# Optimization experiments

Hardware: AMD Instinct MI355X
Metric: run time of the kernel (lower is better)

## Reference

```python
import jax, jax.numpy as jnp
import numpy as np

H = 4        # nhead
TEMP = 0.1   # temperature
TOP_K = 5
SHAPE_EPS = 1e-5


def _ln(x, g, b):
    m = x.mean(-1, keepdims=True)
    v = ((x - m) ** 2).mean(-1, keepdims=True)
    return (x - m) / jnp.sqrt(v + SHAPE_EPS) * g + b


def _mha(x, Wqkv, bqkv, Wo, bo):
    B, L, D = x.shape
    Dh = D // H
    qkv = x @ Wqkv.T + bqkv                     # [B,L,3D]
    q, k, v = jnp.split(qkv, 3, axis=-1)
    q = q.reshape(B, L, H, Dh)
    k = k.reshape(B, L, H, Dh)
    v = v.reshape(B, L, H, Dh)
    att = jnp.einsum('bqhd,bkhd->bhqk', q, k) * (1.0 / np.sqrt(Dh))
    att = jax.nn.softmax(att, axis=-1)
    o = jnp.einsum('bhqk,bkhd->bqhd', att, v).reshape(B, L, D)
    return o @ Wo.T + bo


def _pattern_encoder(x, cls_token, Wqkv, bqkv, Wo, bo, ln1_g, ln1_b,
                     W1, b1, W2, b2, ln2_g, ln2_b, proj_W, proj_b, proj_g, proj_bb):
    B, L, D = x.shape
    h = jnp.concatenate([jnp.broadcast_to(cls_token, (B, 1, D)), x], axis=1)  # [B,L+1,D]
    for i in range(Wqkv.shape[0]):  # num_layers=2, post-norm (PyTorch default)
        a = _mha(h, Wqkv[i], bqkv[i], Wo[i], bo[i])
        h = _ln(h + a, ln1_g[i], ln1_b[i])
        f = jax.nn.gelu(h @ W1[i].T + b1[i], approximate=False) @ W2[i].T + b2[i]
        h = _ln(h + f, ln2_g[i], ln2_b[i])
    cls_out = h[:, 0, :]
    return _ln(cls_out @ proj_W.T + proj_b, proj_g, proj_bb)  # [B,d_repr]


def _value_encoder(xm, vW1, vb1, v_g, v_b, vW2, vb2):
    hh = _ln(xm @ vW1.T + vb1, v_g, v_b)
    return jax.nn.gelu(hh, approximate=False) @ vW2.T + vb2


def setup_inputs() -> dict:
    B, L, D, DR, N, P, NL = 64, 512, 512, 128, 10000, 96, 2
    key = jax.random.key(0)
    ks = jax.random.split(key, 16)
    sc = 0.02
    inp = {
        'query': jax.random.normal(ks[0], (B, L, D), jnp.float32),
        'memory_keys': jax.random.normal(ks[1], (N, DR), jnp.float32),
        'memory_values': jax.random.normal(ks[2], (N, P, D), jnp.float32),
        'cls_token': jax.random.normal(ks[3], (1, 1, D), jnp.float32) * sc,
        'Wqkv': jax.random.normal(ks[4], (NL, 3 * D, D), jnp.float32) * sc,
        'bqkv': jnp.zeros((NL, 3 * D), jnp.float32),
        'Wo': jax.random.normal(ks[5], (NL, D, D), jnp.float32) * sc,
        'bo': jnp.zeros((NL, D), jnp.float32),
        'ln1_g': jnp.ones((NL, D), jnp.float32),
        'ln1_b': jnp.zeros((NL, D), jnp.float32),
        'W1': jax.random.normal(ks[6], (NL, 2 * D, D), jnp.float32) * sc,
        'b1': jnp.zeros((NL, 2 * D), jnp.float32),
        'W2': jax.random.normal(ks[7], (NL, D, 2 * D), jnp.float32) * sc,
        'b2': jnp.zeros((NL, D), jnp.float32),
        'ln2_g': jnp.ones((NL, D), jnp.float32),
        'ln2_b': jnp.zeros((NL, D), jnp.float32),
        'proj_W': jax.random.normal(ks[8], (DR, D), jnp.float32) * sc,
        'proj_b': jnp.zeros((DR,), jnp.float32),
        'proj_g': jnp.ones((DR,), jnp.float32),
        'proj_bb': jnp.zeros((DR,), jnp.float32),
        'vW1': jax.random.normal(ks[9], (DR, D), jnp.float32) * sc,
        'vb1': jnp.zeros((DR,), jnp.float32),
        'v_g': jnp.ones((DR,), jnp.float32),
        'v_b': jnp.zeros((DR,), jnp.float32),
        'vW2': jax.random.normal(ks[10], (DR, DR), jnp.float32) * sc,
        'vb2': jnp.zeros((DR,), jnp.float32),
        'shape_w': jnp.float32(0.5),
    }
    return inp


def reference(query, memory_keys, memory_values, cls_token, Wqkv, bqkv, Wo, bo,
              ln1_g, ln1_b, W1, b1, W2, b2, ln2_g, ln2_b,
              proj_W, proj_b, proj_g, proj_bb, vW1, vb1, v_g, v_b, vW2, vb2, shape_w):
    q_repr = _pattern_encoder(query, cls_token, Wqkv, bqkv, Wo, bo, ln1_g, ln1_b,
                              W1, b1, W2, b2, ln2_g, ln2_b, proj_W, proj_b, proj_g, proj_bb)
    q_val = _value_encoder(query.mean(axis=1), vW1, vb1, v_g, v_b, vW2, vb2)
    qk = shape_w * q_repr + (1.0 - shape_w) * q_val              # [B,DR]
    # squared euclidean distance, expanded form (same math as sum((a-b)^2))
    d = ((qk ** 2).sum(-1)[:, None]
         - 2.0 * qk @ memory_keys.T
         + (memory_keys ** 2).sum(-1)[None, :])                  # [B,N]
    sim = -d / TEMP
    top_scores, top_idx = jax.lax.top_k(sim, TOP_K)              # [B,K]
    weights = jax.nn.softmax(top_scores, axis=-1)
    retrieved = memory_values[top_idx]                           # [B,K,P,D]
    return retrieved, weights
```

## Files before the change

kernel.cpp:

```cpp
#include <hip/hip_runtime.h>
#include <math.h>

#define B_    64
#define LQ    512
#define LC    513
#define DD    512
#define HH    4
#define DH    128
#define DRr   128
#define NKEYS 10000
#define PP    96
#define TOPK  5
#define MROWS (B_*LC)
#define VTSTRIDE 544

typedef __attribute__((ext_vector_type(8))) short short8v;
typedef __attribute__((ext_vector_type(4))) float f32x4;

static __device__ __forceinline__ float gelu_exact(float x) {
    return 0.5f * x * (1.0f + erff(x * 0.70710678118654752440f));
}

static __device__ __forceinline__ unsigned short f2bf(float x) {
    union { float f; unsigned u; } v; v.f = x;
    unsigned r = v.u + 0x7fff + ((v.u >> 16) & 1);
    return (unsigned short)(r >> 16);
}
static __device__ __forceinline__ float bf2f(unsigned short h) {
    union { float f; unsigned u; } v; v.u = ((unsigned)h) << 16;
    return v.f;
}
static __device__ __forceinline__ void split_bf(float x, unsigned short& hi, unsigned short& lo) {
    hi = f2bf(x);
    lo = f2bf(x - bf2f(hi));
}

static __device__ __forceinline__ void gload16(const unsigned short* g, unsigned short* l) {
    __builtin_amdgcn_global_load_lds(
        (const __attribute__((address_space(1))) unsigned*)g,
        (__attribute__((address_space(3))) unsigned*)l, 16, 0, 0);
}

__global__ __launch_bounds__(256)
void split_kernel(const float* __restrict__ x, unsigned short* __restrict__ hi,
                  unsigned short* __restrict__ lo, int n4)
{
    int i = blockIdx.x * blockDim.x + threadIdx.x;
    if (i >= n4) return;
    float4 v = ((const float4*)x)[i];
    unsigned short h0,h1,h2,h3,l0,l1,l2,l3;
    split_bf(v.x,h0,l0); split_bf(v.y,h1,l1); split_bf(v.z,h2,l2); split_bf(v.w,h3,l3);
    ((uint2*)hi)[i] = make_uint2((unsigned)h0 | ((unsigned)h1 << 16), (unsigned)h2 | ((unsigned)h3 << 16));
    ((uint2*)lo)[i] = make_uint2((unsigned)l0 | ((unsigned)l1 << 16), (unsigned)l2 | ((unsigned)l3 << 16));
}

__global__ __launch_bounds__(128)
void concat_cls(const float* __restrict__ query, const float* __restrict__ cls,
                float* __restrict__ h, unsigned short* __restrict__ h_hi,
                unsigned short* __restrict__ h_lo)
{
    int row = blockIdx.x;
    int t = threadIdx.x;
    int b = row / LC, r = row - b * LC;
    const float* src = (r == 0) ? cls : (query + ((size_t)b * LQ + (r - 1)) * DD);
    float4 v = *(const float4*)(src + t * 4);
    *(float4*)(h + (size_t)row * DD + t * 4) = v;
    unsigned short hs[4], ls[4];
    split_bf(v.x, hs[0], ls[0]); split_bf(v.y, hs[1], ls[1]);
    split_bf(v.z, hs[2], ls[2]); split_bf(v.w, hs[3], ls[3]);
    size_t o = (size_t)row * DD + t * 4;
    ((uint2*)(h_hi))[o >> 2] = make_uint2((unsigned)hs[0] | ((unsigned)hs[1]<<16),
                                          (unsigned)hs[2] | ((unsigned)hs[3]<<16));
    ((uint2*)(h_lo))[o >> 2] = make_uint2((unsigned)ls[0] | ((unsigned)ls[1]<<16),
                                          (unsigned)ls[2] | ((unsigned)ls[3]<<16));
}

#define BM 128
#define BN 128
#define BK 32

#define MFMA16(a, b, c) __builtin_amdgcn_mfma_f32_16x16x32_bf16(a, b, c, 0, 0, 0)

template<int MODE>
__global__ __launch_bounds__(256)
void gemm3(const unsigned short* __restrict__ Ahi, const unsigned short* __restrict__ Alo,
           const unsigned short* __restrict__ Whi, const unsigned short* __restrict__ Wlo,
           const float* __restrict__ bias, const float* __restrict__ res,
           float* __restrict__ Cf, unsigned short* __restrict__ Chi,
           unsigned short* __restrict__ Clo, unsigned short* __restrict__ Vhi,
           unsigned short* __restrict__ Vlo, int M, int N, int K)
{
    __shared__ __align__(16) unsigned short LAh[4096];
    __shared__ __align__(16) unsigned short LAl[4096];
    __shared__ __align__(16) unsigned short LBh[4096];
    __shared__ __align__(16) unsigned short LBl[4096];

    const int t = threadIdx.x;
    const int lane = t & 63, w = t >> 6;
    const int wr = w >> 1, wc = w & 1;
    const int row0 = blockIdx.x * BM, col0 = blockIdx.y * BN;

    const int srow = t >> 2;
    const int sg   = t & 3;
    const int glog = sg ^ ((srow >> 1) & 3);
    int ar0 = row0 + srow;      if (ar0 >= M) ar0 = M - 1;
    int ar1 = row0 + srow + 64; if (ar1 >= M) ar1 = M - 1;
    const size_t aoff0 = (size_t)ar0 * K + glog * 8;
    const size_t aoff1 = (size_t)ar1 * K + glog * 8;
    const size_t boff0 = (size_t)(col0 + srow) * K + glog * 8;
    const size_t boff1 = (size_t)(col0 + srow + 64) * K + glog * 8;
    const int ldso0 = t * 8;
    const int ldso1 = t * 8 + 2048;

    f32x4 acc[4][4];
    #pragma unroll
    for (int m = 0; m < 4; m++)
        #pragma unroll
        for (int n = 0; n < 4; n++) { acc[m][n][0]=0.f; acc[m][n][1]=0.f; acc[m][n][2]=0.f; acc[m][n][3]=0.f; }

    const int c = lane & 15;
    const int g = lane >> 4;
    const int gs = (g ^ ((c >> 1) & 3)) * 8;

    const int KT = K / BK;
    for (int kt = 0; kt < KT; kt++) {
        const int k0 = kt * BK;
        __syncthreads();
        gload16(Ahi + aoff0 + k0, &LAh[ldso0]);
        gload16(Ahi + aoff1 + k0, &LAh[ldso1]);
        gload16(Alo + aoff0 + k0, &LAl[ldso0]);
        gload16(Alo + aoff1 + k0, &LAl[ldso1]);
        gload16(Whi + boff0 + k0, &LBh[ldso0]);
        gload16(Whi + boff1 + k0, &LBh[ldso1]);
        gload16(Wlo + boff0 + k0, &LBl[ldso0]);
        gload16(Wlo + boff1 + k0, &LBl[ldso1]);
        __syncthreads();

        short8v ah[4], al[4], bh[4], bl[4];
        #pragma unroll
        for (int m = 0; m < 4; m++) {
            int off = (wr * 64 + m * 16 + c) * 32 + gs;
            ah[m] = *(const short8v*)&LAh[off];
            al[m] = *(const short8v*)&LAl[off];
        }
        #pragma unroll
        for (int n = 0; n < 4; n++) {
            int off = (wc * 64 + n * 16 + c) * 32 + gs;
            bh[n] = *(const short8v*)&LBh[off];
            bl[n] = *(const short8v*)&LBl[off];
        }

        #pragma unroll
        for (int m = 0; m < 4; m++)
            #pragma unroll
            for (int n = 0; n < 4; n++) {
                acc[m][n] = MFMA16(ah[m], bh[n], acc[m][n]);
                acc[m][n] = MFMA16(al[m], bh[n], acc[m][n]);
                acc[m][n] = MFMA16(ah[m], bl[n], acc[m][n]);
            }
    }

    #pragma unroll
    for (int m = 0; m < 4; m++) {
        int rb = row0 + wr * 64 + m * 16 + (lane >> 4) * 4;
        #pragma unroll
        for (int n = 0; n < 4; n++) {
            int cc = col0 + wc * 64 + n * 16 + c;
            float bcol = bias[cc];
            #pragma unroll
            for (int r = 0; r < 4; r++) {
                int row = rb + r;
                if (row < M) {
                    float v = acc[m][n][r] + bcol;
                    if (MODE == 1) v += res[(size_t)row * N + cc];
                    if (MODE == 2) {
                        v = gelu_exact(v);
                        unsigned short hv, lv;
                        split_bf(v, hv, lv);
                        Chi[(size_t)row * N + cc] = hv;
                        Clo[(size_t)row * N + cc] = lv;
                    } else if (MODE == 3) {
                        unsigned short hv, lv;
                        split_bf(v, hv, lv);
                        if (cc < 1024) {
                            Chi[(size_t)row * 1024 + cc] = hv;
                            Clo[(size_t)row * 1024 + cc] = lv;
                        } else {
                            int da = cc - 1024, hh = da >> 7, dd = da & 127;
                            int bb = row / LC, ll = row - bb * LC;
                            size_t vi = ((size_t)((bb * HH + hh) * DH + dd)) * VTSTRIDE + ll;
                            Vhi[vi] = hv; Vlo[vi] = lv;
                        }
                    } else {
                        Cf[(size_t)row * N + cc] = v;
                    }
                }
            }
        }
    }
}

#define AQT 64
#define AKT 32
#define NKT2 17
__global__ __launch_bounds__(256)
void attn_mfma(const unsigned short* __restrict__ qkhi, const unsigned short* __restrict__ qklo,
               const unsigned short* __restrict__ vthi, const unsigned short* __restrict__ vtlo,
               unsigned short* __restrict__ ohi, unsigned short* __restrict__ olo)
{
    __shared__ __align__(16) unsigned short SM[24064];
    #define KH(r,d) SM[(r)*136 + (d)]
    #define KL(r,d) SM[4352 + (r)*136 + (d)]
    #define VH(d,k) SM[8704 + (d)*40 + (k)]
    #define VL(d,k) SM[13824 + (d)*40 + (k)]
    #define PH(r,k) SM[18944 + (r)*40 + (k)]
    #define PL(r,k) SM[21504 + (r)*40 + (k)]
    #define OS(r,d) SM[(r)*136 + (d)]

    const int t = threadIdx.x;
    const int lane = t & 63, w = t >> 6;
    const int qt = blockIdx.x, h = blockIdx.y, b = blockIdx.z;
    const int q0 = qt * AQT;
    const int c = lane & 15, g = lane >> 4;
    const float SCALE = 0.08838834764831845f;

    short8v qh[4], ql[4];
    {
        int qrow = b * LC + q0 + w * 16 + c;
        if (qrow > MROWS - 1) qrow = MROWS - 1;
        const unsigned short* bh_ = qkhi + (size_t)qrow * 1024 + h * DH;
        const unsigned short* bl_ = qklo + (size_t)qrow * 1024 + h * DH;
        #pragma unroll
        for (int ks = 0; ks < 4; ks++) {
            qh[ks] = *(const short8v*)(bh_ + ks * 32 + g * 8);
            ql[ks] = *(const short8v*)(bl_ + ks * 32 + g * 8);
        }
    }

    float m_r[4], l_r[4];
    #pragma unroll
    for (int r = 0; r < 4; r++) { m_r[r] = -INFINITY; l_r[r] = 0.f; }
    f32x4 acc_o[8];
    #pragma unroll
    for (int n = 0; n < 8; n++) { acc_o[n][0]=0.f; acc_o[n][1]=0.f; acc_o[n][2]=0.f; acc_o[n][3]=0.f; }

    const int skr = t >> 3, skd = (t & 7) * 16;
    const int svd = t >> 1, svk = (t & 1) * 16;

    for (int kt = 0; kt < NKT2; kt++) {
        __syncthreads();
        {
            int krow = b * LC + kt * AKT + skr;
            if (krow > MROWS - 1) krow = MROWS - 1;
            const unsigned short* kb  = qkhi + (size_t)krow * 1024 + 512 + h * DH + skd;
            const unsigned short* kbl = qklo + (size_t)krow * 1024 + 512 + h * DH + skd;
            *(short8v*)&KH(skr, skd)     = *(const short8v*)kb;
            *(short8v*)&KH(skr, skd + 8) = *(const short8v*)(kb + 8);
            *(short8v*)&KL(skr, skd)     = *(const short8v*)kbl;
            *(short8v*)&KL(skr, skd + 8) = *(const short8v*)(kbl + 8);
            const unsigned short* vb  = vthi + ((size_t)((b * HH + h) * DH + svd)) * VTSTRIDE + kt * AKT + svk;
            const unsigned short* vbl = vtlo + ((size_t)((b * HH + h) * DH + svd)) * VTSTRIDE + kt * AKT + svk;
            *(short8v*)&VH(svd, svk)     = *(const short8v*)vb;
            *(short8v*)&VH(svd, svk + 8) = *(const short8v*)(vb + 8);
            *(short8v*)&VL(svd, svk)     = *(const short8v*)vbl;
            *(short8v*)&VL(svd, svk + 8) = *(const short8v*)(vbl + 8);
        }
        __syncthreads();

        f32x4 s[2];
        s[0][0]=s[0][1]=s[0][2]=s[0][3]=0.f;
        s[1][0]=s[1][1]=s[1][2]=s[1][3]=0.f;
        #pragma unroll
        for (int n = 0; n < 2; n++) {
            #pragma unroll
            for (int ks = 0; ks < 4; ks++) {
                short8v kh = *(const short8v*)&KH(n * 16 + c, ks * 32 + g * 8);
                short8v kl = *(const short8v*)&KL(n * 16 + c, ks * 32 + g * 8);
                s[n] = MFMA16(qh[ks], kh, s[n]);
                s[n] = MFMA16(ql[ks], kh, s[n]);
                s[n] = MFMA16(qh[ks], kl, s[n]);
            }
        }

        #pragma unroll
        for (int n = 0; n < 2; n++) {
            bool oob = (kt * 32 + n * 16 + c) >= LC;
            #pragma unroll
            for (int r = 0; r < 4; r++) {
                float sv = s[n][r] * SCALE;
                s[n][r] = oob ? -INFINITY : sv;
            }
        }

        float alpha[4], p0v[4], p1v[4];
        #pragma unroll
        for (int r = 0; r < 4; r++) {
            float rm = fmaxf(s[0][r], s[1][r]);
            #pragma unroll
            for (int off = 1; off < 16; off <<= 1) rm = fmaxf(rm, __shfl_xor(rm, off));
            float mn = fmaxf(m_r[r], rm);
            float p0 = expf(s[0][r] - mn);
            float p1 = expf(s[1][r] - mn);
            float ts = p0 + p1;
            #pragma unroll
            for (int off = 1; off < 16; off <<= 1) ts += __shfl_xor(ts, off);
            float al = expf(m_r[r] - mn);
            m_r[r] = mn;
            l_r[r] = al * l_r[r] + ts;
            alpha[r] = al;
            p0v[r] = p0; p1v[r] = p1;
        }

        #pragma unroll
        for (int n = 0; n < 8; n++)
            #pragma unroll
            for (int r = 0; r < 4; r++) acc_o[n][r] *= alpha[r];

        #pragma unroll
        for (int r = 0; r < 4; r++) {
            unsigned short ph, pl;
            split_bf(p0v[r], ph, pl);
            PH(w * 16 + g * 4 + r, c) = ph;
            PL(w * 16 + g * 4 + r, c) = pl;
            split_bf(p1v[r], ph, pl);
            PH(w * 16 + g * 4 + r, 16 + c) = ph;
            PL(w * 16 + g * 4 + r, 16 + c) = pl;
        }
        __syncthreads();

        short8v pah = *(const short8v*)&PH(w * 16 + c, g * 8);
        short8v pal = *(const short8v*)&PL(w * 16 + c, g * 8);
        #pragma unroll
        for (int n = 0; n < 8; n++) {
            short8v vh = *(const short8v*)&VH(n * 16 + c, g * 8);
            short8v vl = *(const short8v*)&VL(n * 16 + c, g * 8);
            acc_o[n] = MFMA16(pah, vh, acc_o[n]);
            acc_o[n] = MFMA16(pal, vh, acc_o[n]);
            acc_o[n] = MFMA16(pah, vl, acc_o[n]);
        }
    }

    float inv[4];
    #pragma unroll
    for (int r = 0; r < 4; r++) inv[r] = 1.0f / l_r[r];

    const int orow = t >> 2, oc0 = (t & 3) * 32;
    #pragma unroll
    for (int pass = 0; pass < 2; pass++) {
        __syncthreads();
        #pragma unroll
        for (int n = 0; n < 8; n++)
            #pragma unroll
            for (int r = 0; r < 4; r++) {
                float v = acc_o[n][r] * inv[r];
                unsigned short hv, lv;
                split_bf(v, hv, lv);
                OS(w * 16 + g * 4 + r, n * 16 + c) = pass ? lv : hv;
            }
        __syncthreads();
        int grow = q0 + orow;
        if (grow < LC) {
            unsigned short* dst = (pass ? olo : ohi) + ((size_t)(b * LC + grow)) * DD + h * DH + oc0;
            #pragma unroll
            for (int u = 0; u < 4; u++)
                *(short8v*)(dst + u * 8) = *(const short8v*)&OS(orow, oc0 + u * 8);
        }
    }
    #undef KH
    #undef KL
    #undef VH
    #undef VL
    #undef PH
    #undef PL
    #undef OS
}

__global__ __launch_bounds__(128)
void ln512(const float* __restrict__ X, const float* __restrict__ g,
           const float* __restrict__ bb, float* __restrict__ Y,
           unsigned short* __restrict__ Yhi, unsigned short* __restrict__ Ylo)
{
    __shared__ float red[2];
    int row = blockIdx.x, t = threadIdx.x;
    const float* x = X + (size_t)row * DD;
    float4 v = *(const float4*)(x + t * 4);
    float s = v.x + v.y + v.z + v.w;
    #pragma unroll
    for (int off = 1; off < 64; off <<= 1) s += __shfl_xor(s, off);
    if ((t & 63) == 0) red[t >> 6] = s;
    __syncthreads();
    float mean = (red[0] + red[1]) * (1.0f / 512.0f);
    __syncthreads();
    float d0 = v.x - mean, d1 = v.y - mean, d2 = v.z - mean, d3 = v.w - mean;
    float s2 = d0 * d0 + d1 * d1 + d2 * d2 + d3 * d3;
    #pragma unroll
    for (int off = 1; off < 64; off <<= 1) s2 += __shfl_xor(s2, off);
    if ((t & 63) == 0) red[t >> 6] = s2;
    __syncthreads();
    float var = (red[0] + red[1]) * (1.0f / 512.0f);
    float rstd = 1.0f / sqrtf(var + 1e-5f);
    float4 gv = *(const float4*)(g + t * 4);
    float4 bv = *(const float4*)(bb + t * 4);
    float4 ov;
    ov.x = d0 * rstd * gv.x + bv.x;
    ov.y = d1 * rstd * gv.y + bv.y;
    ov.z = d2 * rstd * gv.z + bv.z;
    ov.w = d3 * rstd * gv.w + bv.w;
    size_t o = (size_t)row * DD + t * 4;
    *(float4*)(Y + o) = ov;
    unsigned short hs[4], ls[4];
    split_bf(ov.x, hs[0], ls[0]); split_bf(ov.y, hs[1], ls[1]);
    split_bf(ov.z, hs[2], ls[2]); split_bf(ov.w, hs[3], ls[3]);
    ((uint2*)Yhi)[o >> 2] = make_uint2((unsigned)hs[0] | ((unsigned)hs[1]<<16),
                                       (unsigned)hs[2] | ((unsigned)hs[3]<<16));
    ((uint2*)Ylo)[o >> 2] = make_uint2((unsigned)ls[0] | ((unsigned)ls[1]<<16),
                                       (unsigned)ls[2] | ((unsigned)ls[3]<<16));
}

__global__ __launch_bounds__(128)
void mean_part(const float* __restrict__ query, float* __restrict__ part)
{
    int b = blockIdx.x, ch = blockIdx.y, t = threadIdx.x;
    const float* base = query + ((size_t)b * LQ + ch * 64) * DD + t * 4;
    float ax = 0.f, ay = 0.f, az = 0.f, aw = 0.f;
    for (int l = 0; l < 64; l++) {
        float4 v = *(const float4*)(base + (size_t)l * DD);
        ax += v.x; ay += v.y; az += v.z; aw += v.w;
    }
    *(float4*)(part + ((size_t)(b * 8 + ch)) * DD + t * 4) = make_float4(ax, ay, az, aw);
}

__global__ __launch_bounds__(128)
void mean_fin(const float* __restrict__ part, float* __restrict__ xm)
{
    int b = blockIdx.x, t = threadIdx.x;
    float ax = 0.f, ay = 0.f, az = 0.f, aw = 0.f;
    #pragma unroll
    for (int ch = 0; ch < 8; ch++) {
        float4 v = *(const float4*)(part + ((size_t)(b * 8 + ch)) * DD + t * 4);
        ax += v.x; ay += v.y; az += v.z; aw += v.w;
    }
    *(float4*)(xm + (size_t)b * DD + t * 4) =
        make_float4(ax * (1.f/512.f), ay * (1.f/512.f), az * (1.f/512.f), aw * (1.f/512.f));
}

static __device__ __forceinline__ float block128_sum(float x, float* red, int t) {
    #pragma unroll
    for (int off = 1; off < 64; off <<= 1) x += __shfl_xor(x, off);
    if ((t & 63) == 0) red[t >> 6] = x;
    __syncthreads();
    float r = red[0] + red[1];
    __syncthreads();
    return r;
}

__global__ __launch_bounds__(128)
void proj_ln(const float* __restrict__ h, const float* __restrict__ pW, const float* __restrict__ pb,
             const float* __restrict__ pg, const float* __restrict__ pbb, float* __restrict__ q_repr)
{
    __shared__ float xs[DD];
    __shared__ float red[2];
    int b = blockIdx.x, t = threadIdx.x;
    *(float4*)&xs[t * 4] = *(const float4*)(h + (size_t)(b * LC) * DD + t * 4);
    __syncthreads();
    const float* w = pW + (size_t)t * DD;
    float acc = pb[t];
    for (int k = 0; k < DD; k += 4) {
        float4 a = *(const float4*)&xs[k];
        float4 ww = *(const float4*)(w + k);
        acc += a.x * ww.x + a.y * ww.y + a.z * ww.z + a.w * ww.w;
    }
    float mean = block128_sum(acc, red, t) * (1.f / 128.f);
    float dx = acc - mean;
    float var = block128_sum(dx * dx, red, t) * (1.f / 128.f);
    float rstd = 1.0f / sqrtf(var + 1e-5f);
    q_repr[(size_t)b * DRr + t] = dx * rstd * pg[t] + pbb[t];
}

__global__ __launch_bounds__(128)
void venc(const float* __restrict__ xm, const float* __restrict__ vW1, const float* __restrict__ vb1,
          const float* __restrict__ vg, const float* __restrict__ vb,
          const float* __restrict__ vW2, const float* __restrict__ vb2,
          float* __restrict__ q_val)
{
    __shared__ float xs[DD];
    __shared__ float hg[DRr];
    __shared__ float red[2];
    int b = blockIdx.x, t = threadIdx.x;
    *(float4*)&xs[t * 4] = *(const float4*)(xm + (size_t)b * DD + t * 4);
    __syncthreads();
    const float* w = vW1 + (size_t)t * DD;
    float acc = vb1[t];
    for (int k = 0; k < DD; k += 4) {
        float4 a = *(const float4*)&xs[k];
        float4 ww = *(const float4*)(w + k);
        acc += a.x * ww.x + a.y * ww.y + a.z * ww.z + a.w * ww.w;
    }
    float mean = block128_sum(acc, red, t) * (1.f / 128.f);
    float dx = acc - mean;
    float var = block128_sum(dx * dx, red, t) * (1.f / 128.f);
    float rstd = 1.0f / sqrtf(var + 1e-5f);
    float hn = dx * rstd * vg[t] + vb[t];
    hg[t] = gelu_exact(hn);
    __syncthreads();
    const float* w2 = vW2 + (size_t)t * DRr;
    float acc2 = vb2[t];
    for (int k = 0; k < DRr; k += 4) {
        float4 a = *(const float4*)&hg[k];
        float4 ww = *(const float4*)(w2 + k);
        acc2 += a.x * ww.x + a.y * ww.y + a.z * ww.z + a.w * ww.w;
    }
    q_val[(size_t)b * DRr + t] = acc2;
}

__global__ void combine_qk(const float* __restrict__ qr, const float* __restrict__ qv,
                           const float* __restrict__ swp, float* __restrict__ qk)
{
    int i = blockIdx.x * blockDim.x + threadIdx.x;
    if (i < B_ * DRr) {
        float sw = swp[0];
        qk[i] = sw * qr[i] + (1.f - sw) * qv[i];
    }
}

#define SIMCH 10
__global__ __launch_bounds__(256)
void sim_kernel(const float* __restrict__ qk, const float* __restrict__ mkeys, float* __restrict__ sim)
{
    __shared__ float qs[DRr];
    int b = blockIdx.x, ch = blockIdx.y, t = threadIdx.x;
    if (t < DRr) qs[t] = qk[(size_t)b * DRr + t];
    __syncthreads();
    float qn = 0.f;
    #pragma unroll 8
    for (int i = 0; i < DRr; i++) qn += qs[i] * qs[i];
    int n0 = ch * (NKEYS / SIMCH), n1 = n0 + (NKEYS / SIMCH);
    for (int n = n0 + t; n < n1; n += 256) {
        const float* kr = mkeys + (size_t)n * DRr;
        float dot = 0.f, kn = 0.f;
        #pragma unroll 8
        for (int i = 0; i < DRr; i += 4) {
            float4 kv = *(const float4*)(kr + i);
            dot += qs[i] * kv.x + qs[i + 1] * kv.y + qs[i + 2] * kv.z + qs[i + 3] * kv.w;
            kn  += kv.x * kv.x + kv.y * kv.y + kv.z * kv.z + kv.w * kv.w;
        }
        float d = qn - 2.f * dot + kn;
        sim[(size_t)b * NKEYS + n] = -d / 0.1f;
    }
}

static __device__ __forceinline__ void topk_insert(float* v, int* id, float x, int n) {
    bool better = (x > v[TOPK - 1]) || (x == v[TOPK - 1] && n < id[TOPK - 1]);
    if (better) {
        v[TOPK - 1] = x; id[TOPK - 1] = n;
        #pragma unroll
        for (int k = TOPK - 1; k > 0; k--) {
            bool sw = (v[k] > v[k - 1]) || (v[k] == v[k - 1] && id[k] < id[k - 1]);
            if (!sw) break;
            float tv = v[k]; v[k] = v[k - 1]; v[k - 1] = tv;
            int ti = id[k]; id[k] = id[k - 1]; id[k - 1] = ti;
        }
    }
}

__global__ __launch_bounds__(256)
void topk_kernel(const float* __restrict__ sim, int* __restrict__ topidx, float* __restrict__ wout)
{
    __shared__ float sv[256][TOPK];
    __shared__ int   si[256][TOPK];
    int b = blockIdx.x, t = threadIdx.x;
    float v[TOPK]; int id[TOPK];
    #pragma unroll
    for (int k = 0; k < TOPK; k++) { v[k] = -INFINITY; id[k] = 0x7fffffff; }
    for (int n = t; n < NKEYS; n += 256) {
        topk_insert(v, id, sim[(size_t)b * NKEYS + n], n);
    }
    #pragma unroll
    for (int k = 0; k < TOPK; k++) { sv[t][k] = v[k]; si[t][k] = id[k]; }
    for (int strd = 128; strd >= 1; strd >>= 1) {
        __syncthreads();
        if (t < strd) {
            #pragma unroll
            for (int k = 0; k < TOPK; k++) topk_insert(v, id, sv[t + strd][k], si[t + strd][k]);
            #pragma unroll
            for (int k = 0; k < TOPK; k++) { sv[t][k] = v[k]; si[t][k] = id[k]; }
        }
    }
    if (t == 0) {
        float m = v[0];
        float e[TOPK]; float sum = 0.f;
        #pragma unroll
        for (int k = 0; k < TOPK; k++) { e[k] = expf(v[k] - m); sum += e[k]; }
        #pragma unroll
        for (int k = 0; k < TOPK; k++) {
            wout[(size_t)b * TOPK + k] = e[k] / sum;
            topidx[b * TOPK + k] = id[k];
        }
    }
}

__global__ __launch_bounds__(128)
void gather_kernel(const float* __restrict__ mv, const int* __restrict__ topidx, float* __restrict__ out)
{
    int blk = blockIdx.x;
    int b = blk / (TOPK * PP);
    int rem = blk - b * (TOPK * PP);
    int k = rem / PP;
    int p = rem - k * PP;
    int idx = topidx[b * TOPK + k];
    const float4* src = (const float4*)(mv + ((size_t)idx * PP + p) * DD);
    float4* dst = (float4*)(out + (size_t)blk * DD);
    dst[threadIdx.x] = src[threadIdx.x];
}

extern "C" void kernel_launch(void* const* d_in, const int* in_sizes, int n_in,
                              void* d_out, int out_size, void* d_ws, size_t ws_size,
                              hipStream_t stream) {
    const float* query = (const float*)d_in[0];
    const float* mkeys = (const float*)d_in[1];
    const float* mvals = (const float*)d_in[2];
    const float* cls   = (const float*)d_in[3];
    const float* Wqkv  = (const float*)d_in[4];
    const float* bqkv  = (const float*)d_in[5];
    const float* Wo    = (const float*)d_in[6];
    const float* bo    = (const float*)d_in[7];
    const float* ln1g  = (const float*)d_in[8];
    const float* ln1b  = (const float*)d_in[9];
    const float* W1    = (const float*)d_in[10];
    const float* b1    = (const float*)d_in[11];
    const float* W2    = (const float*)d_in[12];
    const float* b2    = (const float*)d_in[13];
    const float* ln2g  = (const float*)d_in[14];
    const float* ln2b  = (const float*)d_in[15];
    const float* pW    = (const float*)d_in[16];
    const float* pb    = (const float*)d_in[17];
    const float* pg    = (const float*)d_in[18];
    const float* pbb   = (const float*)d_in[19];
    const float* vW1   = (const float*)d_in[20];
    const float* vb1   = (const float*)d_in[21];
    const float* vg    = (const float*)d_in[22];
    const float* vb    = (const float*)d_in[23];
    const float* vW2   = (const float*)d_in[24];
    const float* vb2   = (const float*)d_in[25];
    const float* swp   = (const float*)d_in[26];
    float* out = (float*)d_out;

    float* ws    = (float*)d_ws;
    float* h     = ws;
    float* preln = h + (size_t)MROWS * DD;
    unsigned short* h_hi  = (unsigned short*)(preln + (size_t)MROWS * DD);
    unsigned short* h_lo  = h_hi  + (size_t)MROWS * DD;
    unsigned short* mid_hi = h_lo + (size_t)MROWS * DD;
    unsigned short* mid_lo = mid_hi + (size_t)MROWS * 1024;
    unsigned short* qkhi  = mid_lo + (size_t)MROWS * 1024;
    unsigned short* qklo  = qkhi  + (size_t)MROWS * 1024;
    unsigned short* vthi  = qklo  + (size_t)MROWS * 1024;
    unsigned short* vtlo  = vthi  + (size_t)32768 * VTSTRIDE;
    unsigned short* wq_hi = vtlo  + (size_t)32768 * VTSTRIDE;
    unsigned short* wq_lo = wq_hi + (size_t)2 * 1536 * DD;
    unsigned short* wo_hi = wq_lo + (size_t)2 * 1536 * DD;
    unsigned short* wo_lo = wo_hi + (size_t)2 * DD * DD;
    unsigned short* w1_hi = wo_lo + (size_t)2 * DD * DD;
    unsigned short* w1_lo = w1_hi + (size_t)2 * 1024 * DD;
    unsigned short* w2_hi = w1_lo + (size_t)2 * 1024 * DD;
    unsigned short* w2_lo = w2_hi + (size_t)2 * DD * 1024;
    float* xm   = (float*)(w2_lo + (size_t)2 * DD * 1024);
    float* qval = xm   + (size_t)B_ * DD;
    float* qrep = qval + (size_t)B_ * DRr;
    float* qkc  = qrep + (size_t)B_ * DRr;
    float* simb = qkc  + (size_t)B_ * DRr;
    int*   tidx = (int*)(simb + (size_t)B_ * NKEYS);
    float* mpart = (float*)(tidx + 512);
    (void)ws_size; (void)in_sizes; (void)n_in; (void)out_size;

    {
        int n4;
        n4 = 2 * 1536 * DD / 4;
        split_kernel<<<(n4 + 255) / 256, 256, 0, stream>>>(Wqkv, wq_hi, wq_lo, n4);
        n4 = 2 * DD * DD / 4;
        split_kernel<<<(n4 + 255) / 256, 256, 0, stream>>>(Wo, wo_hi, wo_lo, n4);
        n4 = 2 * 1024 * DD / 4;
        split_kernel<<<(n4 + 255) / 256, 256, 0, stream>>>(W1, w1_hi, w1_lo, n4);
        n4 = 2 * DD * 1024 / 4;
        split_kernel<<<(n4 + 255) / 256, 256, 0, stream>>>(W2, w2_hi, w2_lo, n4);
    }

    concat_cls<<<MROWS, 128, 0, stream>>>(query, cls, h, h_hi, h_lo);

    for (int l = 0; l < 2; l++) {
        const unsigned short* wqh = wq_hi + (size_t)l * 1536 * DD;
        const unsigned short* wql = wq_lo + (size_t)l * 1536 * DD;
        const unsigned short* woh = wo_hi + (size_t)l * DD * DD;
        const unsigned short* wol = wo_lo + (size_t)l * DD * DD;
        const unsigned short* w1h = w1_hi + (size_t)l * 1024 * DD;
        const unsigned short* w1l = w1_lo + (size_t)l * 1024 * DD;
        const unsigned short* w2h = w2_hi + (size_t)l * DD * 1024;
        const unsigned short* w2l = w2_lo + (size_t)l * DD * 1024;
        const float* bq  = bqkv + (size_t)l * 1536;
        const float* bol = bo   + (size_t)l * DD;
        const float* g1  = ln1g + (size_t)l * DD;
        const float* be1 = ln1b + (size_t)l * DD;
        const float* b1l = b1   + (size_t)l * 1024;
        const float* b2l = b2   + (size_t)l * DD;
        const float* g2  = ln2g + (size_t)l * DD;
        const float* be2 = ln2b + (size_t)l * DD;

        gemm3<3><<<dim3(257, 12), 256, 0, stream>>>(h_hi, h_lo, wqh, wql, bq, nullptr,
                                                    nullptr, qkhi, qklo, vthi, vtlo,
                                                    MROWS, 1536, DD);
        attn_mfma<<<dim3(9, HH, B_), 256, 0, stream>>>(qkhi, qklo, vthi, vtlo, h_hi, h_lo);
        gemm3<1><<<dim3(257, 4), 256, 0, stream>>>(h_hi, h_lo, woh, wol, bol, h,
                                                   preln, nullptr, nullptr, nullptr, nullptr,
                                                   MROWS, DD, DD);
        ln512<<<MROWS, 128, 0, stream>>>(preln, g1, be1, h, h_hi, h_lo);
        gemm3<2><<<dim3(257, 8), 256, 0, stream>>>(h_hi, h_lo, w1h, w1l, b1l, nullptr,
                                                   nullptr, mid_hi, mid_lo, nullptr, nullptr,
                                                   MROWS, 1024, DD);
        gemm3<1><<<dim3(257, 4), 256, 0, stream>>>(mid_hi, mid_lo, w2h, w2l, b2l, h,
                                                   preln, nullptr, nullptr, nullptr, nullptr,
                                                   MROWS, DD, 1024);
        ln512<<<MROWS, 128, 0, stream>>>(preln, g2, be2, h, h_hi, h_lo);
    }

    proj_ln<<<B_, 128, 0, stream>>>(h, pW, pb, pg, pbb, qrep);
    mean_part<<<dim3(B_, 8), 128, 0, stream>>>(query, mpart);
    mean_fin<<<B_, 128, 0, stream>>>(mpart, xm);
    venc<<<B_, 128, 0, stream>>>(xm, vW1, vb1, vg, vb, vW2, vb2, qval);
    combine_qk<<<(B_ * DRr + 255) / 256, 256, 0, stream>>>(qrep, qval, swp, qkc);
    sim_kernel<<<dim3(B_, SIMCH), 256, 0, stream>>>(qkc, mkeys, simb);
    topk_kernel<<<B_, 256, 0, stream>>>(simb, tidx, out + (size_t)B_ * TOPK * PP * DD);
    gather_kernel<<<B_ * TOPK * PP, 128, 0, stream>>>(mvals, tidx, out);
}
```

Measured before the change: 2.499 ms.

## Switch GEMM to 32x32x16 MFMA tiles and interleave V hi/lo stores

The split-bf16 GEMM now uses 32x32x16 MFMA instructions, with 2x2 fragments per wave instead of 4x4 16x16 fragments. The LDS swizzle and epilogue row mapping are changed to match the new fragment layout. The larger MFMA shape should cut LDS fragment reads per FLOP and raise matrix-core efficiency. Separately, the transposed V hi/lo halves are written as one packed 32-bit word to a single buffer, and the attention kernel unpacks them. This replaces two scattered 16-bit stores with one, at the cost of extra bit shuffling in attention.

```diff
diff --git a/kernel.cpp b/kernel.cpp
--- a/kernel.cpp
+++ b/kernel.cpp
@@ -16,6 +16,7 @@
 
 typedef __attribute__((ext_vector_type(8))) short short8v;
 typedef __attribute__((ext_vector_type(4))) float f32x4;
+typedef __attribute__((ext_vector_type(16))) float f32x16;
 
 static __device__ __forceinline__ float gelu_exact(float x) {
     return 0.5f * x * (1.0f + erff(x * 0.70710678118654752440f));
@@ -79,7 +80,7 @@
 #define BN 128
 #define BK 32
 
-#define MFMA16(a, b, c) __builtin_amdgcn_mfma_f32_16x16x32_bf16(a, b, c, 0, 0, 0)
+#define MFMA32(a, b, c) __builtin_amdgcn_mfma_f32_32x32x16_bf16(a, b, c, 0, 0, 0)
 
 template<int MODE>
 __global__ __launch_bounds__(256)
@@ -87,8 +88,8 @@
            const unsigned short* __restrict__ Whi, const unsigned short* __restrict__ Wlo,
            const float* __restrict__ bias, const float* __restrict__ res,
            float* __restrict__ Cf, unsigned short* __restrict__ Chi,
-           unsigned short* __restrict__ Clo, unsigned short* __restrict__ Vhi,
-           unsigned short* __restrict__ Vlo, int M, int N, int K)
+           unsigned short* __restrict__ Clo, unsigned* __restrict__ Vix,
+           int M, int N, int K)
 {
     __shared__ __align__(16) unsigned short LAh[4096];
     __shared__ __align__(16) unsigned short LAl[4096];
@@ -102,7 +103,7 @@
 
     const int srow = t >> 2;
     const int sg   = t & 3;
-    const int glog = sg ^ ((srow >> 1) & 3);
+    const int glog = sg ^ (srow & 3);
     int ar0 = row0 + srow;      if (ar0 >= M) ar0 = M - 1;
     int ar1 = row0 + srow + 64; if (ar1 >= M) ar1 = M - 1;
     const size_t aoff0 = (size_t)ar0 * K + glog * 8;
@@ -112,15 +113,17 @@
     const int ldso0 = t * 8;
     const int ldso1 = t * 8 + 2048;
 
-    f32x4 acc[4][4];
-    #pragma unroll
-    for (int m = 0; m < 4; m++)
-        #pragma unroll
-        for (int n = 0; n < 4; n++) { acc[m][n][0]=0.f; acc[m][n][1]=0.f; acc[m][n][2]=0.f; acc[m][n][3]=0.f; }
-
-    const int c = lane & 15;
-    const int g = lane >> 4;
-    const int gs = (g ^ ((c >> 1) & 3)) * 8;
+    f32x16 acc[2][2];
+    #pragma unroll
+    for (int m = 0; m < 2; m++)
+        #pragma unroll
+        for (int n = 0; n < 2; n++)
+            #pragma unroll
+            for (int i = 0; i < 16; i++) acc[m][n][i] = 0.f;
+
+    const int cl = lane & 31;
+    const int kg = lane >> 5;
+    const int cl3 = cl & 3;
 
     const int KT = K / BK;
     for (int kt = 0; kt < KT; kt++) {
@@ -136,63 +139,69 @@
         gload16(Wlo + boff1 + k0, &LBl[ldso1]);
         __syncthreads();
 
-        short8v ah[4], al[4], bh[4], bl[4];
-        #pragma unroll
-        for (int m = 0; m < 4; m++) {
-            int off = (wr * 64 + m * 16 + c) * 32 + gs;
-            ah[m] = *(const short8v*)&LAh[off];
-            al[m] = *(const short8v*)&LAl[off];
-        }
-        #pragma unroll
-        for (int n = 0; n < 4; n++) {
-            int off = (wc * 64 + n * 16 + c) * 32 + gs;
-            bh[n] = *(const short8v*)&LBh[off];
-            bl[n] = *(const short8v*)&LBl[off];
-        }
-
-        #pragma unroll
-        for (int m = 0; m < 4; m++)
-            #pragma unroll
-            for (int n = 0; n < 4; n++) {
-                acc[m][n] = MFMA16(ah[m], bh[n], acc[m][n]);
-                acc[m][n] = MFMA16(al[m], bh[n], acc[m][n]);
-                acc[m][n] = MFMA16(ah[m], bl[n], acc[m][n]);
+        #pragma unroll
+        for (int ks = 0; ks < 2; ks++) {
+            const int blkswz = ((ks * 2 + kg) ^ cl3) * 8;
+            short8v ah[2], al[2], bh[2], bl[2];
+            #pragma unroll
+            for (int m = 0; m < 2; m++) {
+                int off = (wr * 64 + m * 32 + cl) * 32 + blkswz;
+                ah[m] = *(const short8v*)&LAh[off];
+                al[m] = *(const short8v*)&LAl[off];
             }
-    }
-
-    #pragma unroll
-    for (int m = 0; m < 4; m++) {
-        int rb = row0 + wr * 64 + m * 16 + (lane >> 4) * 4;
-        #pragma unroll
-        for (int n = 0; n < 4; n++) {
-            int cc = col0 + wc * 64 + n * 16 + c;
-            float bcol = bias[cc];
-            #pragma unroll
-            for (int r = 0; r < 4; r++) {
-                int row = rb + r;
-                if (row < M) {
-                    float v = acc[m][n][r] + bcol;
-                    if (MODE == 1) v += res[(size_t)row * N + cc];
-                    if (MODE == 2) {
-                        v = gelu_exact(v);
-                        unsigned short hv, lv;
-                        split_bf(v, hv, lv);
-                        Chi[(size_t)row * N + cc] = hv;
-                        Clo[(size_t)row * N + cc] = lv;
-                    } else if (MODE == 3) {
-                        unsigned short hv, lv;
-                        split_bf(v, hv, lv);
-                        if (cc < 1024) {
-                            Chi[(size_t)row * 1024 + cc] = hv;
-                            Clo[(size_t)row * 1024 + cc] = lv;
+            #pragma unroll
+            for (int n = 0; n < 2; n++) {
+                int off = (wc * 64 + n * 32 + cl) * 32 + blkswz;
+                bh[n] = *(const short8v*)&LBh[off];
+                bl[n] = *(const short8v*)&LBl[off];
+            }
+            #pragma unroll
+            for (int m = 0; m < 2; m++)
+                #pragma unroll
+                for (int n = 0; n < 2; n++) {
+                    acc[m][n] = MFMA32(ah[m], bh[n], acc[m][n]);
+                    acc[m][n] = MFMA32(al[m], bh[n], acc[m][n]);
+                    acc[m][n] = MFMA32(ah[m], bl[n], acc[m][n]);
+                }
+        }
+    }
+
+    #pragma unroll
+    for (int m = 0; m < 2; m++) {
+        const int rb = row0 + wr * 64 + m * 32 + 4 * kg;
+        #pragma unroll
+        for (int n = 0; n < 2; n++) {
+            const int cc = col0 + wc * 64 + n * 32 + cl;
+            const float bcol = bias[cc];
+            #pragma unroll
+            for (int q = 0; q < 4; q++) {
+                #pragma unroll
+                for (int r = 0; r < 4; r++) {
+                    int row = rb + 8 * q + r;
+                    if (row < M) {
+                        float v = acc[m][n][q * 4 + r] + bcol;
+                        if (MODE == 1) v += res[(size_t)row * N + cc];
+                        if (MODE == 2) {
+                            v = gelu_exact(v);
+                            unsigned short hv, lv;
+                            split_bf(v, hv, lv);
+                            Chi[(size_t)row * N + cc] = hv;
+                            Clo[(size_t)row * N + cc] = lv;
+                        } else if (MODE == 3) {
+                            unsigned short hv, lv;
+                            split_bf(v, hv, lv);
+                            if (cc < 1024) {
+                                Chi[(size_t)row * 1024 + cc] = hv;
+                                Clo[(size_t)row * 1024 + cc] = lv;
+                            } else {
+                                int da = cc - 1024, hh = da >> 7, dd = da & 127;
+                                int bb = row / LC, ll = row - bb * LC;
+                                size_t vi = ((size_t)((bb * HH + hh) * DH + dd)) * VTSTRIDE + ll;
+                                Vix[vi] = (unsigned)hv | ((unsigned)lv << 16);
+                            }
                         } else {
-                            int da = cc - 1024, hh = da >> 7, dd = da & 127;
-                            int bb = row / LC, ll = row - bb * LC;
-                            size_t vi = ((size_t)((bb * HH + hh) * DH + dd)) * VTSTRIDE + ll;
-                            Vhi[vi] = hv; Vlo[vi] = lv;
+                            Cf[(size_t)row * N + cc] = v;
                         }
-                    } else {
-                        Cf[(size_t)row * N + cc] = v;
                     }
                 }
             }
@@ -203,9 +212,10 @@
 #define AQT 64
 #define AKT 32
 #define NKT2 17
+#define MFMA16(a, b, c) __builtin_amdgcn_mfma_f32_16x16x32_bf16(a, b, c, 0, 0, 0)
 __global__ __launch_bounds__(256)
 void attn_mfma(const unsigned short* __restrict__ qkhi, const unsigned short* __restrict__ qklo,
-               const unsigned short* __restrict__ vthi, const unsigned short* __restrict__ vtlo,
+               const unsigned* __restrict__ vtx,
                unsigned short* __restrict__ ohi, unsigned short* __restrict__ olo)
 {
     __shared__ __align__(16) unsigned short SM[24064];
@@ -258,12 +268,32 @@
             *(short8v*)&KH(skr, skd + 8) = *(const short8v*)(kb + 8);
             *(short8v*)&KL(skr, skd)     = *(const short8v*)kbl;
             *(short8v*)&KL(skr, skd + 8) = *(const short8v*)(kbl + 8);
-            const unsigned short* vb  = vthi + ((size_t)((b * HH + h) * DH + svd)) * VTSTRIDE + kt * AKT + svk;
-            const unsigned short* vbl = vtlo + ((size_t)((b * HH + h) * DH + svd)) * VTSTRIDE + kt * AKT + svk;
-            *(short8v*)&VH(svd, svk)     = *(const short8v*)vb;
-            *(short8v*)&VH(svd, svk + 8) = *(const short8v*)(vb + 8);
-            *(short8v*)&VL(svd, svk)     = *(const short8v*)vbl;
-            *(short8v*)&VL(svd, svk + 8) = *(const short8v*)(vbl + 8);
+            const unsigned* vb = vtx + ((size_t)((b * HH + h) * DH + svd)) * VTSTRIDE + kt * AKT + svk;
+            uint4 a0 = *(const uint4*)(vb);
+            uint4 a1 = *(const uint4*)(vb + 4);
+            uint4 a2 = *(const uint4*)(vb + 8);
+            uint4 a3 = *(const uint4*)(vb + 12);
+            uint4 hA, hB, lA, lB;
+            hA.x = (a0.x & 0xffffu) | (a0.y << 16);
+            hA.y = (a0.z & 0xffffu) | (a0.w << 16);
+            hA.z = (a1.x & 0xffffu) | (a1.y << 16);
+            hA.w = (a1.z & 0xffffu) | (a1.w << 16);
+            hB.x = (a2.x & 0xffffu) | (a2.y << 16);
+            hB.y = (a2.z & 0xffffu) | (a2.w << 16);
+            hB.z = (a3.x & 0xffffu) | (a3.y << 16);
+            hB.w = (a3.z & 0xffffu) | (a3.w << 16);
+            lA.x = (a0.x >> 16) | (a0.y & 0xffff0000u);
+            lA.y = (a0.z >> 16) | (a0.w & 0xffff0000u);
+            lA.z = (a1.x >> 16) | (a1.y & 0xffff0000u);
+            lA.w = (a1.z >> 16) | (a1.w & 0xffff0000u);
+            lB.x = (a2.x >> 16) | (a2.y & 0xffff0000u);
+            lB.y = (a2.z >> 16) | (a2.w & 0xffff0000u);
+            lB.z = (a3.x >> 16) | (a3.y & 0xffff0000u);
+            lB.w = (a3.z >> 16) | (a3.w & 0xffff0000u);
+            *(uint4*)&VH(svd, svk)     = hA;
+            *(uint4*)&VH(svd, svk + 8) = hB;
+            *(uint4*)&VL(svd, svk)     = lA;
+            *(uint4*)&VL(svd, svk + 8) = lB;
         }
         __syncthreads();
 
@@ -654,9 +684,8 @@
     unsigned short* mid_lo = mid_hi + (size_t)MROWS * 1024;
     unsigned short* qkhi  = mid_lo + (size_t)MROWS * 1024;
     unsigned short* qklo  = qkhi  + (size_t)MROWS * 1024;
-    unsigned short* vthi  = qklo  + (size_t)MROWS * 1024;
-    unsigned short* vtlo  = vthi  + (size_t)32768 * VTSTRIDE;
-    unsigned short* wq_hi = vtlo  + (size_t)32768 * VTSTRIDE;
+    unsigned* vtx         = (unsigned*)(qklo + (size_t)MROWS * 1024);
+    unsigned short* wq_hi = (unsigned short*)(vtx + (size_t)32768 * VTSTRIDE);
     unsigned short* wq_lo = wq_hi + (size_t)2 * 1536 * DD;
     unsigned short* wo_hi = wq_lo + (size_t)2 * 1536 * DD;
     unsigned short* wo_lo = wo_hi + (size_t)2 * DD * DD;
@@ -706,18 +735,18 @@
         const float* be2 = ln2b + (size_t)l * DD;
 
         gemm3<3><<<dim3(257, 12), 256, 0, stream>>>(h_hi, h_lo, wqh, wql, bq, nullptr,
-                                                    nullptr, qkhi, qklo, vthi, vtlo,
+                                                    nullptr, qkhi, qklo, vtx,
                                                     MROWS, 1536, DD);
-        attn_mfma<<<dim3(9, HH, B_), 256, 0, stream>>>(qkhi, qklo, vthi, vtlo, h_hi, h_lo);
+        attn_mfma<<<dim3(9, HH, B_), 256, 0, stream>>>(qkhi, qklo, vtx, h_hi, h_lo);
         gemm3<1><<<dim3(257, 4), 256, 0, stream>>>(h_hi, h_lo, woh, wol, bol, h,
-                                                   preln, nullptr, nullptr, nullptr, nullptr,
+                                                   preln, nullptr, nullptr, nullptr,
                                                    MROWS, DD, DD);
         ln512<<<MROWS, 128, 0, stream>>>(preln, g1, be1, h, h_hi, h_lo);
         gemm3<2><<<dim3(257, 8), 256, 0, stream>>>(h_hi, h_lo, w1h, w1l, b1l, nullptr,
-                                                   nullptr, mid_hi, mid_lo, nullptr, nullptr,
+                                                   nullptr, mid_hi, mid_lo, nullptr,
                                                    MROWS, 1024, DD);
         gemm3<1><<<dim3(257, 4), 256, 0, stream>>>(mid_hi, mid_lo, w2h, w2l, b2l, h,
-                                                   preln, nullptr, nullptr, nullptr, nullptr,
+                                                   preln, nullptr, nullptr, nullptr,
                                                    MROWS, DD, 1024);
         ln512<<<MROWS, 128, 0, stream>>>(preln, g2, be2, h, h_hi, h_lo);
     }
```

Result: faster. 2.430 ms (-2.8%).
